# Kernel optimization log

Measured on AMD Instinct MI355X. Metric: run time of the kernel, lower is better.

Reference implementation:

```python
import jax, jax.numpy as jnp
import numpy as np

B, N, D = 1, 1024, 3584
H, KVH, HD = 28, 4, 128
I = 18944
SEC = [16, 24, 24]  # mrope_section, sums to HD//2
EPS_RMS = 1e-6
EPS_SM = 1e-6


def setup_inputs() -> dict:
    key = jax.random.key(0)
    ks = jax.random.split(key, 16)
    s = 0.02
    return {
        "hidden_states": jax.random.normal(ks[0], (B, N, D), jnp.float32),
        "cos": jax.random.uniform(ks[1], (3, B, N, HD), jnp.float32, -1.0, 1.0),
        "sin": jax.random.uniform(ks[2], (3, B, N, HD), jnp.float32, -1.0, 1.0),
        "prune_mask": jax.random.randint(ks[3], (B, N), 0, 2, jnp.int32),
        "Wq": jax.random.normal(ks[4], (D, H * HD), jnp.float32) * s,
        "bq": jnp.zeros((H * HD,), jnp.float32),
        "Wk": jax.random.normal(ks[5], (D, KVH * HD), jnp.float32) * s,
        "bk": jnp.zeros((KVH * HD,), jnp.float32),
        "Wv": jax.random.normal(ks[6], (D, KVH * HD), jnp.float32) * s,
        "bv": jnp.zeros((KVH * HD,), jnp.float32),
        "Wo": jax.random.normal(ks[7], (H * HD, D), jnp.float32) * s,
        "ln1_w": jnp.ones((D,), jnp.float32),
        "ln2_w": jnp.ones((D,), jnp.float32),
        "Wg": jax.random.normal(ks[8], (D, I), jnp.float32) * s,
        "Wu": jax.random.normal(ks[9], (D, I), jnp.float32) * s,
        "Wd": jax.random.normal(ks[10], (I, D), jnp.float32) * s,
    }


def _rmsnorm(x, w):
    v = jnp.mean(x * x, axis=-1, keepdims=True)
    return x * jax.lax.rsqrt(v + EPS_RMS) * w


def _rotate_half(x):
    h = x.shape[-1] // 2
    return jnp.concatenate([-x[..., h:], x[..., :h]], axis=-1)


def _mrope_select(t):
    # t: (3, B, N, HD) -> (B, 1, N, HD), picking section i from axis i%3
    parts, idx = [], 0
    for i, s in enumerate(SEC * 2):
        parts.append(t[i % 3, :, :, idx:idx + s])
        idx += s
    return jnp.concatenate(parts, axis=-1)[:, None]


def reference(hidden_states, cos, sin, prune_mask, Wq, bq, Wk, bk, Wv, bv, Wo,
              ln1_w, ln2_w, Wg, Wu, Wd):
    x = _rmsnorm(hidden_states, ln1_w)
    q = (x @ Wq + bq).reshape(B, N, H, HD).transpose(0, 2, 1, 3)
    k = (x @ Wk + bk).reshape(B, N, KVH, HD).transpose(0, 2, 1, 3)
    v = (x @ Wv + bv).reshape(B, N, KVH, HD).transpose(0, 2, 1, 3)

    cf, sf = _mrope_select(cos), _mrope_select(sin)
    q = q * cf + _rotate_half(q) * sf
    k = k * cf + _rotate_half(k) * sf

    groups = H // KVH
    k = jnp.repeat(k, groups, axis=1)  # (B,H,N,HD)
    v = jnp.repeat(v, groups, axis=1)

    scores = jnp.einsum("bhqd,bhkd->bhqk", q, k) / np.sqrt(HD).astype(np.float32)
    causal = jnp.tril(jnp.ones((N, N), bool))
    scores = jnp.where(causal, scores, jnp.float32(-1e9))

    # custom prune-masked softmax (softmax_with_mask)
    am = prune_mask.astype(jnp.float32)[:, None, None, :]  # (B,1,1,N)
    eye = jnp.eye(N, dtype=jnp.float32)
    am = am + (1.0 - am) * eye
    mx = jnp.max(scores, axis=-1, keepdims=True)
    e = jnp.exp(scores - mx) * am
    attn = (e + EPS_SM / N) / (jnp.sum(e, axis=-1, keepdims=True) + EPS_SM)

    o = jnp.einsum("bhqk,bhkd->bhqd", attn, v)
    o = o.transpose(0, 2, 1, 3).reshape(B, N, H * HD) @ Wo

    h = hidden_states + o
    y = _rmsnorm(h, ln2_w)
    mlp = (jax.nn.silu(y @ Wg) * (y @ Wu)) @ Wd
    return h + mlp
```

## Files before the change

### kernel.cpp

```cpp
#include <hip/hip_runtime.h>
#include <hip/hip_bf16.h>


#define SEQ   1024
#define DIM   3584
#define NH    28
#define NKVH  4
#define HDIM  128
#define IDIM  18944
#define QKVN  4608
#define GUN   37888

typedef __attribute__((ext_vector_type(8))) __bf16 bf16x8;
typedef __attribute__((ext_vector_type(4))) __bf16 bf16x4;
typedef __attribute__((ext_vector_type(4))) float  f32x4;

static constexpr size_t OFF_WQKVT = 0;
static constexpr size_t OFF_WOT   = OFF_WQKVT + (size_t)QKVN*DIM*2;
static constexpr size_t OFF_WGUT  = OFF_WOT   + (size_t)DIM*DIM*2;
static constexpr size_t OFF_WDT   = OFF_WGUT  + (size_t)GUN*DIM*2;
static constexpr size_t OFF_XB    = OFF_WDT   + (size_t)DIM*IDIM*2;
static constexpr size_t OFF_QKV   = OFF_XB    + (size_t)SEQ*DIM*2;
static constexpr size_t OFF_VT    = OFF_QKV   + (size_t)SEQ*QKVN*2;
static constexpr size_t OFF_VSUMP = OFF_VT    + (size_t)NKVH*HDIM*SEQ*2;
static constexpr size_t OFF_VSUM  = OFF_VSUMP + 4*8*128*4;
static constexpr size_t OFF_BQKV  = OFF_VSUM  + 4*128*4;
static constexpr size_t OFF_OB    = OFF_BQKV  + (size_t)QKVN*4;
static constexpr size_t OFF_HB    = OFF_OB    + (size_t)SEQ*DIM*2;
static constexpr size_t OFF_YB    = OFF_HB    + (size_t)SEQ*DIM*4;
static constexpr size_t OFF_GU    = OFF_YB    + (size_t)SEQ*DIM*2;
static constexpr size_t OFF_PB    = OFF_GU    + (size_t)SEQ*GUN*2;
static constexpr size_t OFF_PART  = OFF_GU;

#define GLL16(gp, lp)                                                        \
  __builtin_amdgcn_global_load_lds(                                         \
      (const __attribute__((address_space(1))) void*)(gp),                  \
      (__attribute__((address_space(3))) void*)(lp), 16, 0, 0)

#define BAR    asm volatile("s_barrier" ::: "memory")
#define SCHEDB __builtin_amdgcn_sched_barrier(0)

__global__ __launch_bounds__(256) void transconv_kernel(
    const float* __restrict__ W, __bf16* __restrict__ WT, int K, int N, int mode)
{
  __shared__ __bf16 t[64][72];
  const int tid = threadIdx.x;
  const int k0 = blockIdx.y * 64, n0 = blockIdx.x * 64;
#pragma unroll
  for (int it = 0; it < 4; ++it) {
    int idx = it * 256 + tid;
    int r = idx >> 4, c4 = idx & 15;
    float4 v = *(const float4*)(W + (size_t)(k0 + r) * N + n0 + c4 * 4);
    t[r][c4 * 4 + 0] = (__bf16)v.x;
    t[r][c4 * 4 + 1] = (__bf16)v.y;
    t[r][c4 * 4 + 2] = (__bf16)v.z;
    t[r][c4 * 4 + 3] = (__bf16)v.w;
  }
  __syncthreads();
#pragma unroll
  for (int it = 0; it < 2; ++it) {
    int idx = it * 256 + tid;
    int r = idx >> 3, c8 = idx & 7;
    bf16x8 o;
#pragma unroll
    for (int i = 0; i < 8; ++i) o[i] = t[c8 * 8 + i][r];
    const int nlog = n0 + r;
    const int orow = (mode == 0) ? nlog
                   : ((nlog >> 4) << 5) + ((mode == 2) ? 16 : 0) + (nlog & 15);
    *(bf16x8*)(WT + (size_t)orow * K + k0 + c8 * 8) = o;
  }
}

__global__ __launch_bounds__(256) void pack_bias_kernel(
    const float* __restrict__ bq, const float* __restrict__ bk,
    const float* __restrict__ bv, float* __restrict__ out)
{
  int i = blockIdx.x * 256 + threadIdx.x;
  if (i < DIM) out[i] = bq[i];
  else if (i < DIM + 512) out[i] = bk[i - DIM];
  else if (i < QKVN) out[i] = bv[i - DIM - 512];
}

__global__ __launch_bounds__(256) void rmsnorm_kernel(
    const float* __restrict__ in, const float* __restrict__ w,
    __bf16* __restrict__ out)
{
  const int row = blockIdx.x;
  const int t = threadIdx.x;
  const float* x = in + (size_t)row * DIM;
  float4 v[4];
  float ss = 0.f;
#pragma unroll
  for (int i = 0; i < 4; ++i) {
    int idx = t + i * 256;
    if (idx < 896) {
      v[i] = ((const float4*)x)[idx];
      ss += v[i].x * v[i].x + v[i].y * v[i].y + v[i].z * v[i].z + v[i].w * v[i].w;
    }
  }
#pragma unroll
  for (int m = 1; m < 64; m <<= 1) ss += __shfl_xor(ss, m);
  __shared__ float red[4];
  if ((t & 63) == 0) red[t >> 6] = ss;
  __syncthreads();
  float tot = red[0] + red[1] + red[2] + red[3];
  float rs = rsqrtf(tot / (float)DIM + 1e-6f);
#pragma unroll
  for (int i = 0; i < 4; ++i) {
    int idx = t + i * 256;
    if (idx < 896) {
      float4 wv = ((const float4*)w)[idx];
      bf16x4 o;
      o[0] = (__bf16)(v[i].x * rs * wv.x);
      o[1] = (__bf16)(v[i].y * rs * wv.y);
      o[2] = (__bf16)(v[i].z * rs * wv.z);
      o[3] = (__bf16)(v[i].w * rs * wv.w);
      *(bf16x4*)(out + (size_t)row * DIM + idx * 4) = o;
    }
  }
}

__global__ __launch_bounds__(256, 2) void gemm_splitk_kernel(
    const __bf16* __restrict__ A, const __bf16* __restrict__ BT,
    float* __restrict__ PART, int M, int N, int K, int Kc, int gridY)
{
  __shared__ __bf16 As[128 * 64];
  __shared__ __bf16 Bs[128 * 64];
  const int tid = threadIdx.x;
  const int l = tid & 63, w = tid >> 6;

  const int nwg = gridDim.x;
  const int bq8 = nwg >> 3, br8 = nwg & 7;
  const int xcd = blockIdx.x & 7, bidx = blockIdx.x >> 3;
  const int wg = (xcd < br8 ? xcd * (bq8 + 1) : br8 * (bq8 + 1) + (xcd - br8) * bq8) + bidx;
  const int tm = wg % gridY;
  const int wg2 = wg / gridY;
  const int gridX = N >> 7;
  const int tn = wg2 % gridX;
  const int ks = wg2 / gridX;
  const int row0 = tm * 128;
  const int col0 = tn * 128;
  const int kbase = ks * Kc;

  const int m0 = (w >> 1) * 64;
  const int n0 = (w & 1) * 64;
  const int lg = l >> 4, lc = l & 15;

  f32x4 acc[4][4] = {};

  size_t aoff[4], boff[4];
  int lbyte[4];
#pragma unroll
  for (int it = 0; it < 4; ++it) {
    const int cbase = (it * 4 + w) * 64;
    const int c = cbase + l;
    const int r = c >> 3, p = c & 7;
    const int b = p ^ (r & 7);
    aoff[it] = (size_t)(row0 + r) * K + kbase + b * 8;
    boff[it] = (size_t)(col0 + r) * K + kbase + b * 8;
    lbyte[it] = cbase * 16;
  }
  const int sw = lc & 7;

  const int ktc = Kc >> 6;
  for (int kt = 0; kt < ktc; ++kt) {
    const int k0 = kt << 6;
#pragma unroll
    for (int it = 0; it < 4; ++it) {
      GLL16(A + aoff[it] + k0, (char*)As + lbyte[it]);
      GLL16(BT + boff[it] + k0, (char*)Bs + lbyte[it]);
    }
    __syncthreads();
#pragma unroll
    for (int s = 0; s < 2; ++s) {
      bf16x8 af[4], bfv[4];
#pragma unroll
      for (int a = 0; a < 4; ++a)
        af[a] = *(const bf16x8*)(As + (m0 + a * 16 + lc) * 64 + ((s * 4 + lg) ^ sw) * 8);
#pragma unroll
      for (int b = 0; b < 4; ++b)
        bfv[b] = *(const bf16x8*)(Bs + (n0 + b * 16 + lc) * 64 + ((s * 4 + lg) ^ sw) * 8);
#pragma unroll
      for (int a = 0; a < 4; ++a)
#pragma unroll
        for (int b = 0; b < 4; ++b)
          acc[a][b] = __builtin_amdgcn_mfma_f32_16x16x32_bf16(af[a], bfv[b], acc[a][b], 0, 0, 0);
    }
    __syncthreads();
  }

  float* P = PART + (size_t)ks * M * N;
  const int lr = lg * 4;
#pragma unroll
  for (int b = 0; b < 4; ++b) {
    const int col = col0 + n0 + b * 16 + lc;
#pragma unroll
    for (int a = 0; a < 4; ++a)
#pragma unroll
      for (int j = 0; j < 4; ++j)
        P[(size_t)(row0 + m0 + a * 16 + lr + j) * N + col] = acc[a][b][j];
  }
}

template<int S, bool BF16OUT, bool BIAS>
__global__ __launch_bounds__(256) void reduce_kernel(
    const float* __restrict__ part, const float* __restrict__ resid,
    const float* __restrict__ bias, void* __restrict__ out, int N, int MN4)
{
  const int i4 = blockIdx.x * 256 + threadIdx.x;
  if (i4 >= MN4) return;
  const size_t base = (size_t)i4 * 4;
  f32x4 s = *(const f32x4*)(part + base);
#pragma unroll
  for (int k = 1; k < S; ++k)
    s += *(const f32x4*)(part + (size_t)k * MN4 * 4 + base);
  if (BIAS) {
    const int col = (int)(base % N);
    s += *(const f32x4*)(bias + col);
  }
  if (resid != nullptr) s += *(const f32x4*)(resid + base);
  if (BF16OUT) {
    bf16x4 o;
#pragma unroll
    for (int j = 0; j < 4; ++j) o[j] = (__bf16)s[j];
    *(bf16x4*)((__bf16*)out + base) = o;
  } else {
    *(f32x4*)((float*)out + base) = s;
  }
}

template<int EPI>
__global__ __launch_bounds__(512, 1) void gemm256_kernel(
    const __bf16* __restrict__ A, const __bf16* __restrict__ BT,
    void* __restrict__ OUT, int M, int N, int K, int Kc, int gridY)
{
  __shared__ int4 lds4[8192];
  char* ldsc = (char*)lds4;
  const int tid = threadIdx.x;
  const int l = tid & 63, w = tid >> 6;
  const int wr = w >> 2, wc = w & 3;
  const int lg = l >> 4, lc = l & 15;

  const int nwg = gridDim.x;
  const int bq8 = nwg >> 3, br8 = nwg & 7;
  const int xcd = blockIdx.x & 7, bidx = blockIdx.x >> 3;
  const int wg = (xcd < br8 ? xcd * (bq8 + 1) : br8 * (bq8 + 1) + (xcd - br8) * bq8) + bidx;
  const int ntn = N >> 8;
  const int wg2 = wg / gridY;
  const int row0 = (wg % gridY) * 256;
  const int col0 = (wg2 % ntn) * 256;
  const int ks = wg2 / ntn;
  const int kbase = ks * Kc;

  size_t aoffj[2], boffj[2];
  int dstj[2];
#pragma unroll
  for (int j = 0; j < 2; ++j) {
    const int c = (j * 8 + w) * 64 + l;
    const int r = c >> 3, p = c & 7;
    const int b = p ^ (r & 7);
    aoffj[j] = (size_t)(row0 + r) * K + kbase + b * 8;
    boffj[j] = (size_t)(col0 + r) * K + kbase + b * 8;
    dstj[j] = (j * 8 + w) * 1024;
  }

#define STG_A(U, KT, BUFB) do {                                              \
    GLL16(A + aoffj[0] + (size_t)(U) * 128 * K + (size_t)(KT) * 64,          \
          ldsc + (BUFB) + (U) * 16384 + dstj[0]);                            \
    GLL16(A + aoffj[1] + (size_t)(U) * 128 * K + (size_t)(KT) * 64,          \
          ldsc + (BUFB) + (U) * 16384 + dstj[1]); } while (0)
#define STG_B(U, KT, BUFB) do {                                              \
    GLL16(BT + boffj[0] + (size_t)(U) * 128 * K + (size_t)(KT) * 64,         \
          ldsc + (BUFB) + 32768 + (U) * 16384 + dstj[0]);                    \
    GLL16(BT + boffj[1] + (size_t)(U) * 128 * K + (size_t)(KT) * 64,         \
          ldsc + (BUFB) + 32768 + (U) * 16384 + dstj[1]); } while (0)

  const int sw = lc & 7;
  const int rdA = (wr * 128 + lc) * 128;
  const int rdB = 32768 + (wc * 64 + lc) * 128;
  const int sk0 = (lg ^ sw) * 16;
  const int sk1 = ((4 | lg) ^ sw) * 16;

  f32x4 acc[8][4] = {};
  bf16x8 af[4][2], bfr[4][2];

#define RD_A4(MH, BUFB) do { _Pragma("unroll")                               \
    for (int mm = 0; mm < 4; ++mm) {                                         \
      af[mm][0] = *(const bf16x8*)(ldsc + (BUFB) + rdA + ((MH) * 4 + mm) * 2048 + sk0); \
      af[mm][1] = *(const bf16x8*)(ldsc + (BUFB) + rdA + ((MH) * 4 + mm) * 2048 + sk1); } } while (0)
#define RD_B2(NL, BUFB) do { _Pragma("unroll")                               \
    for (int nn = 0; nn < 2; ++nn) {                                         \
      bfr[(NL) + nn][0] = *(const bf16x8*)(ldsc + (BUFB) + rdB + ((NL) + nn) * 2048 + sk0); \
      bfr[(NL) + nn][1] = *(const bf16x8*)(ldsc + (BUFB) + rdB + ((NL) + nn) * 2048 + sk1); } } while (0)

#define MFMA16(MH, NL) do { _Pragma("unroll")                                \
    for (int mm = 0; mm < 4; ++mm) { _Pragma("unroll")                       \
      for (int nn = 0; nn < 2; ++nn) {                                       \
        acc[(MH)*4+mm][(NL)+nn] = __builtin_amdgcn_mfma_f32_16x16x32_bf16(   \
            af[mm][0], bfr[(NL)+nn][0], acc[(MH)*4+mm][(NL)+nn], 0, 0, 0);   \
        acc[(MH)*4+mm][(NL)+nn] = __builtin_amdgcn_mfma_f32_16x16x32_bf16(   \
            af[mm][1], bfr[(NL)+nn][1], acc[(MH)*4+mm][(NL)+nn], 0, 0, 0); } } } while (0)

#define PH_MFMA(MH, NL)                                                      \
    BAR; SCHEDB; __builtin_amdgcn_s_setprio(1);                              \
    MFMA16(MH, NL);                                                          \
    __builtin_amdgcn_s_setprio(0); SCHEDB; BAR

  STG_A(0, 0, 0); STG_A(1, 0, 0); STG_B(0, 0, 0); STG_B(1, 0, 0);
  STG_A(0, 1, 65536); STG_A(1, 1, 65536); STG_B(0, 1, 65536); STG_B(1, 1, 65536);
  asm volatile("s_waitcnt vmcnt(8)" ::: "memory");
  BAR;

  const int T = Kc >> 6;
#pragma unroll 1
  for (int i = 0; i < (T >> 1); ++i) {
    const int t0 = 2 * i;
    const int se = (t0 + 2 < T) ? t0 + 2 : 0;
    const int so = (t0 + 3 < T) ? t0 + 3 : 0;
    RD_A4(0, 0); RD_B2(0, 0);
    PH_MFMA(0, 0);
    RD_B2(2, 0);
    PH_MFMA(0, 2);
    RD_A4(1, 0);
    PH_MFMA(1, 2);
    STG_A(0, se, 0); STG_A(1, se, 0);
    asm volatile("s_waitcnt vmcnt(4)" ::: "memory");
    PH_MFMA(1, 0);
    RD_A4(0, 65536); RD_B2(0, 65536);
    STG_B(0, se, 0); STG_B(1, se, 0);
    PH_MFMA(0, 0);
    RD_B2(2, 65536);
    PH_MFMA(0, 2);
    RD_A4(1, 65536);
    PH_MFMA(1, 2);
    STG_A(0, so, 65536); STG_A(1, so, 65536);
    STG_B(0, so, 65536); STG_B(1, so, 65536);
    asm volatile("s_waitcnt vmcnt(8)" ::: "memory");
    PH_MFMA(1, 0);
  }
  asm volatile("s_waitcnt vmcnt(0)" ::: "memory");

  if (EPI == 0) {
    __bf16* PBo = (__bf16*)OUT;
    const int id = N >> 1;
    const int baseq = (col0 + wc * 64) >> 5;
#pragma unroll
    for (int m = 0; m < 8; ++m) {
#pragma unroll
      for (int p = 0; p < 2; ++p) {
        const int gcol = (baseq + p) * 16 + lc;
#pragma unroll
        for (int j = 0; j < 4; ++j) {
          const int row = row0 + wr * 128 + m * 16 + lg * 4 + j;
          const float g = acc[m][2 * p][j];
          const float u = acc[m][2 * p + 1][j];
          const float s = g / (1.f + __expf(-g));
          PBo[(size_t)row * id + gcol] = (__bf16)(s * u);
        }
      }
    }
  } else {
    float* P = (float*)OUT + (size_t)ks * M * N;
#pragma unroll
    for (int m = 0; m < 8; ++m)
#pragma unroll
      for (int n = 0; n < 4; ++n)
#pragma unroll
        for (int j = 0; j < 4; ++j)
          P[(size_t)(row0 + wr * 128 + m * 16 + lg * 4 + j) * N
            + (col0 + wc * 64 + n * 16 + lc)] = acc[m][n][j];
  }
#undef STG_A
#undef STG_B
#undef RD_A4
#undef RD_B2
#undef MFMA16
#undef PH_MFMA
}

__global__ __launch_bounds__(256) void rope_kernel(
    __bf16* __restrict__ qkv, const float* __restrict__ cosb,
    const float* __restrict__ sinb)
{
  const int n = blockIdx.x;
  for (int p = threadIdx.x; p < 32 * 64; p += 256) {
    const int head = p >> 6;
    const int d = p & 63;
    const int src = (d < 16) ? 0 : (d < 40) ? 1 : 2;
    const float* cb = cosb + (size_t)src * SEQ * HDIM + (size_t)n * HDIM;
    const float* sb = sinb + (size_t)src * SEQ * HDIM + (size_t)n * HDIM;
    const float c0 = cb[d], c1 = cb[d + 64];
    const float s0 = sb[d], s1 = sb[d + 64];
    const int col = (head < NH) ? head * HDIM : DIM + (head - NH) * HDIM;
    __bf16* q = qkv + (size_t)n * QKVN + col;
    const float a = (float)q[d];
    const float b = (float)q[d + 64];
    q[d]      = (__bf16)(a * c0 - b * s0);
    q[d + 64] = (__bf16)(b * c1 + a * s1);
  }
}

__global__ __launch_bounds__(256) void vtrans_kernel(
    const __bf16* __restrict__ qkv, __bf16* __restrict__ vT,
    float* __restrict__ vsump)
{
  __shared__ __bf16 t[128][132];
  const int nt = blockIdx.x, kvh = blockIdx.y;
  const int n0 = nt * 128;
  const int tid = threadIdx.x;
#pragma unroll
  for (int it = 0; it < 8; ++it) {
    int idx = it * 256 + tid;
    int nl = idx >> 4, c8 = idx & 15;
    bf16x8 v = *(const bf16x8*)(qkv + (size_t)(n0 + nl) * QKVN + 4096 + kvh * HDIM + c8 * 8);
#pragma unroll
    for (int i = 0; i < 8; ++i) t[nl][c8 * 8 + i] = v[i];
  }
  __syncthreads();
#pragma unroll
  for (int it = 0; it < 8; ++it) {
    int idx = it * 256 + tid;
    int d = idx >> 4, c8 = idx & 15;
    bf16x8 o;
#pragma unroll
    for (int i = 0; i < 8; ++i) o[i] = t[c8 * 8 + i][d];
    *(bf16x8*)(vT + (size_t)(kvh * HDIM + d) * SEQ + n0 + c8 * 8) = o;
  }
  if (tid < 128) {
    float s = 0.f;
    for (int nl = 0; nl < 128; ++nl) s += (float)t[nl][tid];
    vsump[(size_t)(kvh * 8 + nt) * 128 + tid] = s;
  }
}

__global__ __launch_bounds__(512) void vsum_reduce_kernel(
    const float* __restrict__ vsump, float* __restrict__ vsum)
{
  const int idx = threadIdx.x;
  const int kvh = idx >> 7, d = idx & 127;
  float s = 0.f;
#pragma unroll
  for (int nt = 0; nt < 8; ++nt) s += vsump[(size_t)(kvh * 8 + nt) * 128 + d];
  vsum[idx] = s;
}

__global__ __launch_bounds__(256) void attn_kernel(
    const __bf16* __restrict__ qkv, const __bf16* __restrict__ vT,
    const float* __restrict__ vsum, const int* __restrict__ prune,
    __bf16* __restrict__ o)
{
  __shared__ __bf16 plds[4 * 16 * 40];
  const int tid = threadIdx.x;
  const int l = tid & 63, w = tid >> 6;
  const int h = blockIdx.y;
  const int kvh = h / 7;
  const int qt = blockIdx.x;
  const int qbase = qt * 64 + w * 16;
  const int lg = l >> 4, lc = l & 15;
  __bf16* pw = plds + w * (16 * 40);

  bf16x8 qf[4];
#pragma unroll
  for (int s = 0; s < 4; ++s)
    qf[s] = *(const bf16x8*)(qkv + (size_t)(qbase + lc) * QKVN + h * HDIM + s * 32 + lg * 8);

  f32x4 oacc[8] = {};
  float mrun[4] = {-3e38f, -3e38f, -3e38f, -3e38f};
  float lrun[4] = {0.f, 0.f, 0.f, 0.f};

  const int kbEnd = ((qbase + 15) >> 5) + 1;
  for (int kb = 0; kb < kbEnd; ++kb) {
    f32x4 sacc[2] = {};
#pragma unroll
    for (int s = 0; s < 4; ++s) {
#pragma unroll
      for (int c = 0; c < 2; ++c) {
        bf16x8 kf = *(const bf16x8*)(qkv + (size_t)(kb * 32 + c * 16 + lc) * QKVN
                                     + DIM + kvh * HDIM + s * 32 + lg * 8);
        sacc[c] = __builtin_amdgcn_mfma_f32_16x16x32_bf16(qf[s], kf, sacc[c], 0, 0, 0);
      }
    }
    float p[2][4];
    int am[2];
#pragma unroll
    for (int c = 0; c < 2; ++c) {
      const int col = kb * 32 + c * 16 + lc;
      am[c] = (prune[col] != 0) ? 1 : 0;
#pragma unroll
      for (int j = 0; j < 4; ++j) {
        const int row = qbase + lg * 4 + j;
        float sv = sacc[c][j] * 0.08838834764831845f;
        p[c][j] = (col <= row) ? sv : -3e38f;
      }
    }
#pragma unroll
    for (int j = 0; j < 4; ++j) {
      float mx = fmaxf(p[0][j], p[1][j]);
      mx = fmaxf(mx, __shfl_xor(mx, 1));
      mx = fmaxf(mx, __shfl_xor(mx, 2));
      mx = fmaxf(mx, __shfl_xor(mx, 4));
      mx = fmaxf(mx, __shfl_xor(mx, 8));
      const float mnew = fmaxf(mrun[j], mx);
      const float scale = __expf(mrun[j] - mnew);
      mrun[j] = mnew;
      const int row = qbase + lg * 4 + j;
      float rs = 0.f;
#pragma unroll
      for (int c = 0; c < 2; ++c) {
        const int col = kb * 32 + c * 16 + lc;
        float e = __expf(p[c][j] - mnew);
        const int keep = (col == row) ? 1 : am[c];
        e = keep ? e : 0.f;
        p[c][j] = e;
        rs += e;
      }
      rs += __shfl_xor(rs, 1);
      rs += __shfl_xor(rs, 2);
      rs += __shfl_xor(rs, 4);
      rs += __shfl_xor(rs, 8);
      lrun[j] = lrun[j] * scale + rs;
#pragma unroll
      for (int df = 0; df < 8; ++df) oacc[df][j] *= scale;
    }
#pragma unroll
    for (int c = 0; c < 2; ++c)
#pragma unroll
      for (int j = 0; j < 4; ++j)
        pw[(lg * 4 + j) * 40 + c * 16 + lc] = (__bf16)p[c][j];
    bf16x8 pa = *(const bf16x8*)(pw + lc * 40 + lg * 8);
#pragma unroll
    for (int df = 0; df < 8; ++df) {
      bf16x8 vf = *(const bf16x8*)(vT + (size_t)(kvh * HDIM + df * 16 + lc) * SEQ + kb * 32 + lg * 8);
      oacc[df] = __builtin_amdgcn_mfma_f32_16x16x32_bf16(pa, vf, oacc[df], 0, 0, 0);
    }
  }
#pragma unroll
  for (int df = 0; df < 8; ++df) {
    const float vs = vsum[kvh * HDIM + df * 16 + lc];
#pragma unroll
    for (int j = 0; j < 4; ++j) {
      const int row = qbase + lg * 4 + j;
      const float denom = lrun[j] + 1e-6f;
      const float val = (oacc[df][j] + 9.765625e-10f * vs) / denom;
      o[(size_t)row * DIM + h * HDIM + df * 16 + lc] = (__bf16)val;
    }
  }
}

extern "C" void kernel_launch(void* const* d_in, const int* in_sizes, int n_in,
                              void* d_out, int out_size, void* d_ws, size_t ws_size,
                              hipStream_t stream) {
  const float* hidden = (const float*)d_in[0];
  const float* cosb   = (const float*)d_in[1];
  const float* sinb   = (const float*)d_in[2];
  const int*   prune  = (const int*)d_in[3];
  const float* Wq     = (const float*)d_in[4];
  const float* bq     = (const float*)d_in[5];
  const float* Wk     = (const float*)d_in[6];
  const float* bk     = (const float*)d_in[7];
  const float* Wv     = (const float*)d_in[8];
  const float* bv     = (const float*)d_in[9];
  const float* Wo     = (const float*)d_in[10];
  const float* ln1    = (const float*)d_in[11];
  const float* ln2    = (const float*)d_in[12];
  const float* Wg     = (const float*)d_in[13];
  const float* Wu     = (const float*)d_in[14];
  const float* Wd     = (const float*)d_in[15];
  float* out = (float*)d_out;
  char* ws = (char*)d_ws;

  __bf16* WQKVT = (__bf16*)(ws + OFF_WQKVT);
  __bf16* WOT   = (__bf16*)(ws + OFF_WOT);
  __bf16* WGUT  = (__bf16*)(ws + OFF_WGUT);
  __bf16* WDT   = (__bf16*)(ws + OFF_WDT);
  __bf16* XB    = (__bf16*)(ws + OFF_XB);
  __bf16* QKV   = (__bf16*)(ws + OFF_QKV);
  __bf16* VT    = (__bf16*)(ws + OFF_VT);
  float*  VSUMP = (float*)(ws + OFF_VSUMP);
  float*  VSUM  = (float*)(ws + OFF_VSUM);
  float*  BQKV  = (float*)(ws + OFF_BQKV);
  __bf16* OB    = (__bf16*)(ws + OFF_OB);
  float*  HB    = (float*)(ws + OFF_HB);
  __bf16* YB    = (__bf16*)(ws + OFF_YB);
  __bf16* PB    = (__bf16*)(ws + OFF_PB);
  float*  PART  = (float*)(ws + OFF_PART);

  transconv_kernel<<<dim3(DIM / 64, DIM / 64), 256, 0, stream>>>(Wq, WQKVT, DIM, DIM, 0);
  transconv_kernel<<<dim3(512 / 64, DIM / 64), 256, 0, stream>>>(Wk, WQKVT + (size_t)DIM * DIM, DIM, 512, 0);
  transconv_kernel<<<dim3(512 / 64, DIM / 64), 256, 0, stream>>>(Wv, WQKVT + (size_t)4096 * DIM, DIM, 512, 0);
  pack_bias_kernel<<<QKVN / 256, 256, 0, stream>>>(bq, bk, bv, BQKV);
  rmsnorm_kernel<<<SEQ, 256, 0, stream>>>(hidden, ln1, XB);

  gemm_splitk_kernel<<<(QKVN / 128) * (SEQ / 128) * 2, 256, 0, stream>>>(
      XB, WQKVT, PART, SEQ, QKVN, DIM, DIM / 2, SEQ / 128);
  reduce_kernel<2, true, true><<<(SEQ * QKVN / 4 + 255) / 256, 256, 0, stream>>>(
      PART, nullptr, BQKV, QKV, QKVN, SEQ * QKVN / 4);

  rope_kernel<<<SEQ, 256, 0, stream>>>(QKV, cosb, sinb);
  vtrans_kernel<<<dim3(8, NKVH), 256, 0, stream>>>(QKV, VT, VSUMP);
  vsum_reduce_kernel<<<1, 512, 0, stream>>>(VSUMP, VSUM);
  attn_kernel<<<dim3(SEQ / 64, NH), 256, 0, stream>>>(QKV, VT, VSUM, prune, OB);

  transconv_kernel<<<dim3(DIM / 64, DIM / 64), 256, 0, stream>>>(Wo, WOT, DIM, DIM, 0);
  gemm256_kernel<1><<<(DIM / 256) * (SEQ / 256) * 4, 512, 0, stream>>>(
      OB, WOT, PART, SEQ, DIM, DIM, DIM / 4, SEQ / 256);
  reduce_kernel<4, false, false><<<(SEQ * DIM / 4 + 255) / 256, 256, 0, stream>>>(
      PART, hidden, nullptr, HB, DIM, SEQ * DIM / 4);

  rmsnorm_kernel<<<SEQ, 256, 0, stream>>>(HB, ln2, YB);

  transconv_kernel<<<dim3(IDIM / 64, DIM / 64), 256, 0, stream>>>(Wg, WGUT, DIM, IDIM, 1);
  transconv_kernel<<<dim3(IDIM / 64, DIM / 64), 256, 0, stream>>>(Wu, WGUT, DIM, IDIM, 2);
  gemm256_kernel<0><<<(GUN / 256) * (SEQ / 256), 512, 0, stream>>>(
      YB, WGUT, PB, SEQ, GUN, DIM, DIM, SEQ / 256);

  transconv_kernel<<<dim3(DIM / 64, IDIM / 64), 256, 0, stream>>>(Wd, WDT, IDIM, DIM, 0);
  gemm256_kernel<1><<<(DIM / 256) * (SEQ / 256) * 4, 512, 0, stream>>>(
      PB, WDT, PART, SEQ, DIM, IDIM, IDIM / 4, SEQ / 256);
  reduce_kernel<4, false, false><<<(SEQ * DIM / 4 + 255) / 256, 256, 0, stream>>>(
      PART, HB, nullptr, out, DIM, SEQ * DIM / 4);
}
```

Baseline: 986.6 us.

## Restructure GEMM k-loop to two barriers per tile instead of per MFMA phase

Replaces the ping-pong phase structure, which put barriers and sched_barriers around every MFMA block, with a per-tile macro. Each tile reads LDS, runs MFMAs and waits for LDS reads, then issues one barrier before staging the next tile's global loads into the same buffer, with a second barrier after the vmcnt wait. This cuts barrier count and lets the compiler interleave LDS reads with MFMAs. The cost is losing explicit wave interleaving control, and the staging of the next tile is now serialized behind the lgkmcnt wait.

Result: no change. 972.8 us (-1.4%).

```diff
diff --git a/kernel.cpp b/kernel.cpp
--- a/kernel.cpp
+++ b/kernel.cpp
@@ -38,7 +38,6 @@
       (__attribute__((address_space(3))) void*)(lp), 16, 0, 0)
 
 #define BAR    asm volatile("s_barrier" ::: "memory")
-#define SCHEDB __builtin_amdgcn_sched_barrier(0)
 
 __global__ __launch_bounds__(256) void transconv_kernel(
     const float* __restrict__ W, __bf16* __restrict__ WT, int K, int N, int mode)
@@ -301,10 +300,24 @@
         acc[(MH)*4+mm][(NL)+nn] = __builtin_amdgcn_mfma_f32_16x16x32_bf16(   \
             af[mm][1], bfr[(NL)+nn][1], acc[(MH)*4+mm][(NL)+nn], 0, 0, 0); } } } while (0)
 
-#define PH_MFMA(MH, NL)                                                      \
-    BAR; SCHEDB; __builtin_amdgcn_s_setprio(1);                              \
-    MFMA16(MH, NL);                                                          \
-    __builtin_amdgcn_s_setprio(0); SCHEDB; BAR
+#define KTILE(BUFB, TNEXT)                                                   \
+    RD_A4(0, BUFB); RD_B2(0, BUFB);                                          \
+    __builtin_amdgcn_s_setprio(1); MFMA16(0, 0);                             \
+    __builtin_amdgcn_s_setprio(0);                                           \
+    RD_B2(2, BUFB);                                                          \
+    __builtin_amdgcn_s_setprio(1); MFMA16(0, 2);                             \
+    __builtin_amdgcn_s_setprio(0);                                           \
+    RD_A4(1, BUFB);                                                          \
+    __builtin_amdgcn_s_setprio(1); MFMA16(1, 2);                             \
+    __builtin_amdgcn_s_setprio(0);                                           \
+    asm volatile("s_waitcnt lgkmcnt(0)" ::: "memory");                       \
+    BAR;                                    \
+    STG_A(0, TNEXT, BUFB); STG_A(1, TNEXT, BUFB);                            \
+    STG_B(0, TNEXT, BUFB); STG_B(1, TNEXT, BUFB);                            \
+    __builtin_amdgcn_s_setprio(1); MFMA16(1, 0);                             \
+    __builtin_amdgcn_s_setprio(0);                                           \
+    asm volatile("s_waitcnt vmcnt(8)" ::: "memory");  \
+    BAR
 
   STG_A(0, 0, 0); STG_A(1, 0, 0); STG_B(0, 0, 0); STG_B(1, 0, 0);
   STG_A(0, 1, 65536); STG_A(1, 1, 65536); STG_B(0, 1, 65536); STG_B(1, 1, 65536);
@@ -317,26 +330,8 @@
     const int t0 = 2 * i;
     const int se = (t0 + 2 < T) ? t0 + 2 : 0;
     const int so = (t0 + 3 < T) ? t0 + 3 : 0;
-    RD_A4(0, 0); RD_B2(0, 0);
-    PH_MFMA(0, 0);
-    RD_B2(2, 0);
-    PH_MFMA(0, 2);
-    RD_A4(1, 0);
-    PH_MFMA(1, 2);
-    STG_A(0, se, 0); STG_A(1, se, 0);
-    asm volatile("s_waitcnt vmcnt(4)" ::: "memory");
-    PH_MFMA(1, 0);
-    RD_A4(0, 65536); RD_B2(0, 65536);
-    STG_B(0, se, 0); STG_B(1, se, 0);
-    PH_MFMA(0, 0);
-    RD_B2(2, 65536);
-    PH_MFMA(0, 2);
-    RD_A4(1, 65536);
-    PH_MFMA(1, 2);
-    STG_A(0, so, 65536); STG_A(1, so, 65536);
-    STG_B(0, so, 65536); STG_B(1, so, 65536);
-    asm volatile("s_waitcnt vmcnt(8)" ::: "memory");
-    PH_MFMA(1, 0);
+    KTILE(0, se);
+    KTILE(65536, so);
   }
   asm volatile("s_waitcnt vmcnt(0)" ::: "memory");
 
@@ -375,7 +370,7 @@
 #undef RD_A4
 #undef RD_B2
 #undef MFMA16
-#undef PH_MFMA
+#undef KTILE
 }
 
 __global__ __launch_bounds__(256) void rope_kernel(
```
